# Optimization experiments

Hardware: AMD Instinct MI355X
Metric: run time of the kernel (lower is better)

The kernel has to match this reference:

```python
import jax, jax.numpy as jnp
import numpy as np

CROP_SIZE = 8  # config['crop_size']; also >= window_size W=8
N_VIEW, C, H, W = 16, 32, 512, 512
N_TRACK = 2048


def setup_inputs() -> dict:
    key = jax.random.key(0)
    k1, k2, k3 = jax.random.split(key, 3)
    features = jax.random.normal(k1, (1, N_VIEW, C, H, W), dtype=jnp.float32)
    # keypoint (x, y) coords in pixel space, kept away from borders
    sample_points = jax.random.uniform(k2, (1, N_VIEW, N_TRACK, 2), dtype=jnp.float32) * (H - 2 * CROP_SIZE) + CROP_SIZE
    img_idxs = jax.random.randint(k3, (1, N_VIEW, N_TRACK), 0, N_VIEW, dtype=jnp.int64)
    return {"features": features, "sample_points": sample_points, "img_idxs": img_idxs}


def _bilinear_crops(feat, bids, pts, crop_size):
    # feat: [V, C, H, W]; bids: [N] int; pts: [N, 2] (x, y) pixel coords
    # returns [N, crop, crop, C] bilinear samples on a grid spanning
    # [p - r, p + r] with crop_size points (transform_fpcoor=False semantics).
    V, Cc, Hh, Ww = feat.shape
    N = pts.shape[0]
    r = crop_size // 2
    lin = jnp.linspace(-float(r), float(r), crop_size, dtype=pts.dtype)  # [K]
    xs = pts[:, 0:1] + lin  # [N, K]
    ys = pts[:, 1:2] + lin  # [N, K]
    Y = jnp.broadcast_to(ys[:, :, None], (N, crop_size, crop_size))  # rows = y
    X = jnp.broadcast_to(xs[:, None, :], (N, crop_size, crop_size))  # cols = x
    y0 = jnp.floor(Y); x0 = jnp.floor(X)
    wy = (Y - y0)[..., None]  # [N,K,K,1]
    wx = (X - x0)[..., None]
    y0i = y0.astype(jnp.int32); x0i = x0.astype(jnp.int32)
    b = bids.astype(jnp.int32)[:, None, None]  # [N,1,1]

    def gather(yi, xi):
        valid = ((yi >= 0) & (yi < Hh) & (xi >= 0) & (xi < Ww))[..., None]
        yc = jnp.clip(yi, 0, Hh - 1)
        xc = jnp.clip(xi, 0, Ww - 1)
        v = feat[b, :, yc, xc]  # advanced indexing -> [N,K,K,C]
        return v * valid.astype(v.dtype)

    v00 = gather(y0i, x0i)
    v01 = gather(y0i, x0i + 1)
    v10 = gather(y0i + 1, x0i)
    v11 = gather(y0i + 1, x0i + 1)
    return (v00 * (1 - wy) * (1 - wx) + v01 * (1 - wy) * wx
            + v10 * wy * (1 - wx) + v11 * wy * wx)


def reference(features, sample_points, img_idxs):
    # FinePreprocess.forward with sparse=True, enable_rescaled_crop=False
    B, n_view, n_track, _ = sample_points.shape
    feat = features.reshape(B * n_view, features.shape[2], features.shape[3], features.shape[4])
    pts = sample_points.reshape(-1, 2)  # [N, 2]
    bids = img_idxs.reshape(-1)         # [N]
    crops = _bilinear_crops(feat, bids, pts, CROP_SIZE)  # [N, K, K, C]
    N = crops.shape[0]
    # 'n c w h -> n (w h) c' flatten of spatial dims, then split back per view/track
    crops = crops.reshape(N, CROP_SIZE * CROP_SIZE, crops.shape[-1])
    crops = crops.reshape(B, n_view, n_track, CROP_SIZE * CROP_SIZE, crops.shape[-1])
    return crops
```

## Files before the change

### kernel.cpp

```cpp
#include <hip/hip_runtime.h>


#define CROP    8
#define C_CH    32
#define H_DIM   512
#define W_DIM   512
#define HW_SZ   (H_DIM * W_DIM)
#define N_VIEWS 16
#define TPB     4

typedef float f32x4 __attribute__((ext_vector_type(4)));

__device__ __forceinline__ unsigned short f2bf(float f) {
    unsigned int u = __float_as_uint(f);
    u = (u + 0x7fffu + ((u >> 16) & 1u)) >> 16;
    return (unsigned short)u;
}
__device__ __forceinline__ float bf_lo(unsigned int u) {
    return __uint_as_float(u << 16);
}
__device__ __forceinline__ float bf_hi(unsigned int u) {
    return __uint_as_float(u & 0xffff0000u);
}

__global__ __launch_bounds__(256) void chw_to_hwc_bf16(
    const float* __restrict__ feat,
    unsigned short* __restrict__ hwc)
{
    const int xb  = blockIdx.x;
    const int y   = blockIdx.y;
    const int v   = blockIdx.z;
    const int tid = threadIdx.x;

    __shared__ float lds[C_CH][257];

    const int px0 = xb * 256;
    const size_t rbase =
        (size_t)v * C_CH * HW_SZ + (size_t)y * W_DIM + px0;

    #pragma unroll
    for (int c = 0; c < C_CH; ++c)
        lds[c][tid] = feat[rbase + (size_t)c * HW_SZ + tid];

    __syncthreads();

    unsigned short* __restrict__ wbase =
        hwc + (((size_t)v * H_DIM + y) * W_DIM + px0) * C_CH;
    const int c0 = (tid & 7) * 4;

    #pragma unroll
    for (int pp = 0; pp < 8; ++pp) {
        const int px = pp * 32 + (tid >> 3);
        uint2 o;
        o.x = (unsigned int)f2bf(lds[c0 + 0][px]) |
              ((unsigned int)f2bf(lds[c0 + 1][px]) << 16);
        o.y = (unsigned int)f2bf(lds[c0 + 2][px]) |
              ((unsigned int)f2bf(lds[c0 + 3][px]) << 16);
        *reinterpret_cast<uint2*>(wbase + (size_t)px * C_CH + c0) = o;
    }
}

__global__ __launch_bounds__(256, 8) void gather_hwc(
    const unsigned short* __restrict__ hwc,
    const float* __restrict__ pts,
    const int*   __restrict__ bids,
    float*       __restrict__ out,
    int n_tracks)
{
    const int wid  = threadIdx.x >> 6;
    const int lane = threadIdx.x & 63;
    const int t    = blockIdx.x * TPB + wid;
    if (t >= n_tracks) return;

    const int p  = lane >> 3;
    const int c0 = (lane & 7) << 2;

    const float px = pts[2 * t];
    const float py = pts[2 * t + 1];
    const int   b  = bids[t];

    const float linx = (p == 7) ? 4.0f : fmaf((float)p, 8.0f / 7.0f, -4.0f);
    const float X   = px + linx;
    const float x0f = floorf(X);
    const float wx  = X - x0f;
    const int   x0  = (int)x0f;

    const unsigned short* __restrict__ hb =
        hwc + (size_t)b * HW_SZ * C_CH;

    float* __restrict__ obase =
        out + (size_t)t * (CROP * CROP * C_CH) + lane * 4;

    #pragma unroll 2
    for (int r = 0; r < CROP; ++r) {
        const float Y = (r == 0) ? (py - 4.0f)
                      : (r == 7) ? (py + 4.0f)
                      : py + fmaf((float)r, 8.0f / 7.0f, -4.0f);
        const float y0f = floorf(Y);
        const float wy  = Y - y0f;
        const int   y0  = (int)y0f;

        const unsigned short* r0 =
            hb + ((size_t)y0 * W_DIM + x0) * C_CH + c0;
        const unsigned short* r1 = r0 + (size_t)W_DIM * C_CH;

        const uint2 u00 = *reinterpret_cast<const uint2*>(r0);
        const uint2 u01 = *reinterpret_cast<const uint2*>(r0 + C_CH);
        const uint2 u10 = *reinterpret_cast<const uint2*>(r1);
        const uint2 u11 = *reinterpret_cast<const uint2*>(r1 + C_CH);

        const float w00 = (1.0f - wy) * (1.0f - wx);
        const float w01 = (1.0f - wy) * wx;
        const float w10 = wy * (1.0f - wx);
        const float w11 = wy * wx;

        f32x4 o;
        o.x = fmaf(bf_lo(u00.x), w00, fmaf(bf_lo(u01.x), w01,
              fmaf(bf_lo(u10.x), w10, bf_lo(u11.x) * w11)));
        o.y = fmaf(bf_hi(u00.x), w00, fmaf(bf_hi(u01.x), w01,
              fmaf(bf_hi(u10.x), w10, bf_hi(u11.x) * w11)));
        o.z = fmaf(bf_lo(u00.y), w00, fmaf(bf_lo(u01.y), w01,
              fmaf(bf_lo(u10.y), w10, bf_lo(u11.y) * w11)));
        o.w = fmaf(bf_hi(u00.y), w00, fmaf(bf_hi(u01.y), w01,
              fmaf(bf_hi(u10.y), w10, bf_hi(u11.y) * w11)));

        *reinterpret_cast<f32x4*>(obase + r * 256) = o;
    }
}

__global__ __launch_bounds__(256, 8) void fallback_kernel(
    const float* __restrict__ feat,
    const float* __restrict__ pts,
    const int*   __restrict__ bids,
    float*       __restrict__ out,
    int n_tracks)
{
    const int wid  = threadIdx.x >> 6;
    const int lane = threadIdx.x & 63;
    const int t    = blockIdx.x * TPB + wid;
    if (t >= n_tracks) return;

    const int cx = lane >> 3;
    const int c0 = (lane & 7) << 2;

    const float px = pts[2 * t];
    const float py = pts[2 * t + 1];
    const int   b  = bids[t];

    const float linx = (cx == 7) ? 4.0f : fmaf((float)cx, 8.0f / 7.0f, -4.0f);
    const float X   = px + linx;
    const float x0f = floorf(X);
    const float wx  = X - x0f;
    const int   x0  = (int)x0f;

    float* __restrict__ obase =
        out + (size_t)t * (CROP * CROP * C_CH) + lane * 4;

    const float* __restrict__ fp =
        feat + ((size_t)b * C_CH + c0) * HW_SZ + x0;

    #pragma unroll 2
    for (int r = 0; r < CROP; ++r) {
        const float Y = (r == 0) ? (py - 4.0f)
                      : (r == 7) ? (py + 4.0f)
                      : py + fmaf((float)r, 8.0f / 7.0f, -4.0f);
        const float y0f = floorf(Y);
        const float wy  = Y - y0f;
        const int   y0  = (int)y0f;

        const int r0 = y0 * W_DIM;
        const int r1 = r0 + W_DIM;

        const float w00 = (1.0f - wy) * (1.0f - wx);
        const float w01 = (1.0f - wy) * wx;
        const float w10 = wy * (1.0f - wx);
        const float w11 = wy * wx;

        f32x4 o;
        #pragma unroll
        for (int cc = 0; cc < 4; ++cc) {
            const int off = cc * HW_SZ;
            o[cc] = fmaf(fp[r0 + off], w00, fmaf(fp[r0 + off + 1], w01,
                    fmaf(fp[r1 + off], w10, fp[r1 + off + 1] * w11)));
        }
        *reinterpret_cast<f32x4*>(obase + r * 256) = o;
    }
}

extern "C" void kernel_launch(void* const* d_in, const int* in_sizes, int n_in,
                              void* d_out, int out_size, void* d_ws, size_t ws_size,
                              hipStream_t stream) {
    const float* feat = (const float*)d_in[0];
    const float* pts  = (const float*)d_in[1];
    const int*   bids = (const int*)d_in[2];
    float*       out  = (float*)d_out;

    const int n_tracks = in_sizes[2];
    const int blocks   = (n_tracks + TPB - 1) / TPB;

    const size_t hwc_bytes =
        (size_t)N_VIEWS * H_DIM * W_DIM * C_CH * sizeof(unsigned short);

    if (ws_size >= hwc_bytes) {
        unsigned short* hwc = (unsigned short*)d_ws;
        chw_to_hwc_bf16<<<dim3(2, H_DIM, N_VIEWS), 256, 0, stream>>>(feat, hwc);
        gather_hwc<<<blocks, TPB * 64, 0, stream>>>(hwc, pts, bids, out,
                                                    n_tracks);
    } else {
        fallback_kernel<<<blocks, TPB * 64, 0, stream>>>(feat, pts, bids, out,
                                                         n_tracks);
    }
}
```

Before: 250.4 us.

## Reuse shared bilinear source rows across crop rows and use nontemporal memory ops

The gather kernel now loads the union of source rows spanned by the crop (about 10 rows in two batches of six) once per lane. It then picks the two needed rows for each output row with a branch on the floor offset, so overlapping rows between adjacent crop rows are no longer fetched twice. Output stores and the transpose kernel's input loads use nontemporal hints to avoid polluting the cache. This raises register use and relies on the row offset relative to the base falling within the assumed window.

```diff
diff --git a/kernel.cpp b/kernel.cpp
--- a/kernel.cpp
+++ b/kernel.cpp
@@ -40,7 +40,8 @@
 
     #pragma unroll
     for (int c = 0; c < C_CH; ++c)
-        lds[c][tid] = feat[rbase + (size_t)c * HW_SZ + tid];
+        lds[c][tid] =
+            __builtin_nontemporal_load(feat + rbase + (size_t)c * HW_SZ + tid);
 
     __syncthreads();
 
@@ -85,47 +86,78 @@
     const float wx  = X - x0f;
     const int   x0  = (int)x0f;
 
+    const int B0 = (int)floorf(py - 4.0f);
+
+    const size_t rowstride = (size_t)W_DIM * C_CH;
     const unsigned short* __restrict__ hb =
-        hwc + (size_t)b * HW_SZ * C_CH;
+        hwc + (size_t)b * HW_SZ * C_CH + (size_t)B0 * rowstride
+            + (size_t)x0 * C_CH + c0;
 
     float* __restrict__ obase =
         out + (size_t)t * (CROP * CROP * C_CH) + lane * 4;
 
-    #pragma unroll 2
-    for (int r = 0; r < CROP; ++r) {
-        const float Y = (r == 0) ? (py - 4.0f)
-                      : (r == 7) ? (py + 4.0f)
-                      : py + fmaf((float)r, 8.0f / 7.0f, -4.0f);
-        const float y0f = floorf(Y);
-        const float wy  = Y - y0f;
-        const int   y0  = (int)y0f;
-
-        const unsigned short* r0 =
-            hb + ((size_t)y0 * W_DIM + x0) * C_CH + c0;
-        const unsigned short* r1 = r0 + (size_t)W_DIM * C_CH;
-
-        const uint2 u00 = *reinterpret_cast<const uint2*>(r0);
-        const uint2 u01 = *reinterpret_cast<const uint2*>(r0 + C_CH);
-        const uint2 u10 = *reinterpret_cast<const uint2*>(r1);
-        const uint2 u11 = *reinterpret_cast<const uint2*>(r1 + C_CH);
-
-        const float w00 = (1.0f - wy) * (1.0f - wx);
-        const float w01 = (1.0f - wy) * wx;
-        const float w10 = wy * (1.0f - wx);
-        const float w11 = wy * wx;
-
-        f32x4 o;
-        o.x = fmaf(bf_lo(u00.x), w00, fmaf(bf_lo(u01.x), w01,
-              fmaf(bf_lo(u10.x), w10, bf_lo(u11.x) * w11)));
-        o.y = fmaf(bf_hi(u00.x), w00, fmaf(bf_hi(u01.x), w01,
-              fmaf(bf_hi(u10.x), w10, bf_hi(u11.x) * w11)));
-        o.z = fmaf(bf_lo(u00.y), w00, fmaf(bf_lo(u01.y), w01,
-              fmaf(bf_lo(u10.y), w10, bf_lo(u11.y) * w11)));
-        o.w = fmaf(bf_hi(u00.y), w00, fmaf(bf_hi(u01.y), w01,
-              fmaf(bf_hi(u10.y), w10, bf_hi(u11.y) * w11)));
-
-        *reinterpret_cast<f32x4*>(obase + r * 256) = o;
-    }
+    uint2 ua[6], ub[6];
+
+    #pragma unroll
+    for (int j = 0; j < 6; ++j) {
+        ua[j] = *reinterpret_cast<const uint2*>(hb + (size_t)j * rowstride);
+        ub[j] = *reinterpret_cast<const uint2*>(hb + (size_t)j * rowstride + C_CH);
+    }
+
+#define EMIT(r, ja, jb, wy_) do {                                             \
+    const float wy__ = (wy_);                                                 \
+    const float w00 = (1.0f - wy__) * (1.0f - wx);                            \
+    const float w01 = (1.0f - wy__) * wx;                                     \
+    const float w10 = wy__ * (1.0f - wx);                                     \
+    const float w11 = wy__ * wx;                                              \
+    f32x4 o;                                                                  \
+    o.x = fmaf(bf_lo(ua[ja].x), w00, fmaf(bf_lo(ub[ja].x), w01,               \
+          fmaf(bf_lo(ua[jb].x), w10, bf_lo(ub[jb].x) * w11)));                \
+    o.y = fmaf(bf_hi(ua[ja].x), w00, fmaf(bf_hi(ub[ja].x), w01,               \
+          fmaf(bf_hi(ua[jb].x), w10, bf_hi(ub[jb].x) * w11)));                \
+    o.z = fmaf(bf_lo(ua[ja].y), w00, fmaf(bf_lo(ub[ja].y), w01,               \
+          fmaf(bf_lo(ua[jb].y), w10, bf_lo(ub[jb].y) * w11)));                \
+    o.w = fmaf(bf_hi(ua[ja].y), w00, fmaf(bf_hi(ub[ja].y), w01,               \
+          fmaf(bf_hi(ua[jb].y), w10, bf_hi(ub[jb].y) * w11)));                \
+    __builtin_nontemporal_store(o,                                            \
+        reinterpret_cast<f32x4*>(obase + (r) * 256));                         \
+} while (0)
+
+    { const float wy = (py - 4.0f) - (float)B0; EMIT(0, 0, 1, wy); }
+
+#define ROW_P1(r, K) do {                                                     \
+    const float Y   = py + fmaf((float)(r), 8.0f / 7.0f, -4.0f);              \
+    const float y0f = floorf(Y);                                              \
+    const float wy  = Y - y0f;                                                \
+    if ((int)y0f - B0 == (K)) EMIT(r, (K), (K) + 1, wy);                      \
+    else                      EMIT(r, (K) + 1, (K) + 2, wy);                  \
+} while (0)
+
+    ROW_P1(1, 1);
+    ROW_P1(2, 2);
+    ROW_P1(3, 3);
+
+    ua[0] = ua[4]; ub[0] = ub[4];
+    ua[1] = ua[5]; ub[1] = ub[5];
+    #pragma unroll
+    for (int j = 2; j < 6; ++j) {
+        ua[j] = *reinterpret_cast<const uint2*>(hb + (size_t)(j + 4) * rowstride);
+        ub[j] = *reinterpret_cast<const uint2*>(hb + (size_t)(j + 4) * rowstride + C_CH);
+    }
+
+#define ROW_P2(r, K) do {                                                     \
+    const float Y   = py + fmaf((float)(r), 8.0f / 7.0f, -4.0f);              \
+    const float y0f = floorf(Y);                                              \
+    const float wy  = Y - y0f;                                                \
+    if ((int)y0f - B0 == (K) + 4) EMIT(r, (K), (K) + 1, wy);                  \
+    else                          EMIT(r, (K) + 1, (K) + 2, wy);              \
+} while (0)
+
+    ROW_P2(4, 0);
+    ROW_P2(5, 1);
+    ROW_P2(6, 2);
+
+    { const float wy = (py + 4.0f) - (float)(B0 + 8); EMIT(7, 4, 5, wy); }
 }
 
 __global__ __launch_bounds__(256, 8) void fallback_kernel(
```

After: 205.6 us, median of 2. 1.22x faster.
